# Kernel optimization log

Hardware: AMD Instinct MI355X
Metric: run time of the kernel (lower is better)

## Reference

```python
import jax, jax.numpy as jnp
import numpy as np

C = 64           # channels
CPG = 8          # channel_per_group
G = C // CPG     # offset groups = 8
K = 27           # 3x3x3 taps
N, D, H, W = 2, 8, 56, 56


def conv3d(x, w, b=None):
    y = jax.lax.conv_general_dilated(
        x, w, window_strides=(1, 1, 1), padding=[(1, 1)] * 3,
        dimension_numbers=('NCDHW', 'OIDHW', 'NCDHW'))
    if b is not None:
        y = y + b.reshape(1, -1, 1, 1, 1)
    return y


def deform_conv3d(x, off, w, groups):
    # x: [N,C,D,H,W]; off: [N, G*3*27, D,H,W]; w: [O,C,3,3,3]
    n, cin, d, h, wd = x.shape
    cpg = cin // groups
    p = d * h * wd
    off = off.reshape(n, groups, K, 3, d, h, wd)
    # kernel tap displacements in (kd,kh,kw) order, each in {-1,0,1}
    r = jnp.arange(3, dtype=x.dtype) - 1.0
    taps = jnp.stack(jnp.meshgrid(r, r, r, indexing='ij'), axis=-1).reshape(K, 3)
    gd = jnp.arange(d, dtype=x.dtype)[:, None, None]
    gh = jnp.arange(h, dtype=x.dtype)[None, :, None]
    gw = jnp.arange(wd, dtype=x.dtype)[None, None, :]
    # sampling positions [N,G,K,D,H,W]
    pd = gd + taps[:, 0][:, None, None, None] + off[:, :, :, 0]
    ph = gh + taps[:, 1][:, None, None, None] + off[:, :, :, 1]
    pw = gw + taps[:, 2][:, None, None, None] + off[:, :, :, 2]
    d0 = jnp.floor(pd); h0 = jnp.floor(ph); w0 = jnp.floor(pw)
    fd, fh, fw = pd - d0, ph - h0, pw - w0
    d0 = d0.astype(jnp.int32); h0 = h0.astype(jnp.int32); w0 = w0.astype(jnp.int32)
    xflat = x.reshape(n, groups, cpg, p)[:, :, None]  # [N,G,1,Cpg,P]
    acc = jnp.zeros((n, groups, K, cpg, p), x.dtype)
    for cd in (0, 1):
        for ch in (0, 1):
            for cw in (0, 1):
                idd, idh, idw = d0 + cd, h0 + ch, w0 + cw
                wgt = ((fd if cd else 1.0 - fd)
                       * (fh if ch else 1.0 - fh)
                       * (fw if cw else 1.0 - fw))
                valid = ((idd >= 0) & (idd < d) & (idh >= 0) & (idh < h)
                         & (idw >= 0) & (idw < wd)).astype(x.dtype)
                lin = ((jnp.clip(idd, 0, d - 1) * h + jnp.clip(idh, 0, h - 1)) * wd
                       + jnp.clip(idw, 0, wd - 1))
                g = jnp.take_along_axis(xflat, lin.reshape(n, groups, K, 1, p), axis=-1)
                acc = acc + g * (wgt * valid).reshape(n, groups, K, 1, p)
    # [N,G,K,Cpg,P] -> [N,K,C,P]
    vals = acc.transpose(0, 2, 1, 3, 4).reshape(n, K, cin, p)
    out = jnp.einsum('oik,nkip->nop', w.reshape(w.shape[0], cin, K), vals)
    return out.reshape(n, -1, d, h, wd)


def batchnorm(x, gamma, beta, eps=1e-5):
    m = x.mean((0, 2, 3, 4), keepdims=True)
    v = x.var((0, 2, 3, 4), keepdims=True)
    return (gamma.reshape(1, -1, 1, 1, 1) * (x - m) * jax.lax.rsqrt(v + eps)
            + beta.reshape(1, -1, 1, 1, 1))


def setup_inputs() -> dict:
    key = jax.random.key(0)
    ks = jax.random.split(key, 4)
    fan = C * K
    x = jax.random.normal(ks[0], (N, C, D, H, W), jnp.float32)
    w_off = jax.random.normal(ks[1], (G * 3 * K, C, 3, 3, 3), jnp.float32) * 0.01
    b_off = jnp.zeros((G * 3 * K,), jnp.float32)
    w1 = jax.random.normal(ks[2], (C, C, 3, 3, 3), jnp.float32) / np.sqrt(fan).astype(np.float32)
    w2 = jax.random.normal(ks[3], (C, C, 3, 3, 3), jnp.float32) / np.sqrt(fan).astype(np.float32)
    return dict(x=x, w_off=w_off, b_off=b_off, w1=w1,
                gamma1=jnp.ones((C,), jnp.float32), beta1=jnp.zeros((C,), jnp.float32),
                w2=w2, b2=jnp.zeros((C,), jnp.float32),
                gamma2=jnp.ones((C,), jnp.float32), beta2=jnp.zeros((C,), jnp.float32))


def reference(x, w_off, b_off, w1, gamma1, beta1, w2, b2, gamma2, beta2):
    residual = x
    off = conv3d(x, w_off, b_off)
    out = deform_conv3d(x, off, w1, G)
    out = jax.nn.relu(batchnorm(out, gamma1, beta1))
    out = conv3d(out, w2, b2)
    out = batchnorm(out, gamma2, beta2) + residual
    return jax.nn.relu(out)
```

## Files before the change

### kernel.cpp

```cpp
#include <hip/hip_runtime.h>
#include <hip/hip_bf16.h>

#define N_ 2
#define C_ 64
#define D_ 8
#define H_ 56
#define W_ 56
#define HW_ (H_*W_)
#define P_ (D_*HW_)
#define G_ 8
#define CPG_ 8
#define K_ 27
#define CO_OFF_ 648
#define MP_ 768
#define KK_ 1728
#define KB_ (KK_*2)

typedef __attribute__((ext_vector_type(8))) short shortx8;
typedef __attribute__((ext_vector_type(4))) float floatx4;
#define AS1 __attribute__((address_space(1)))
#define AS3 __attribute__((address_space(3)))

__device__ inline float b2f(unsigned short u) {
    union { unsigned u; float f; } x; x.u = ((unsigned)u) << 16; return x.f;
}
__device__ inline unsigned short f2b(float f) {
    union { float f; unsigned u; } x; x.f = f;
    unsigned r = (x.u + 0x7fffu + ((x.u >> 16) & 1u)) >> 16;
    return (unsigned short)r;
}
__device__ inline float lof(unsigned u) { union { unsigned u; float f; } x; x.u = u << 16; return x.f; }
__device__ inline float hif(unsigned u) { union { unsigned u; float f; } x; x.u = u & 0xffff0000u; return x.f; }
__device__ inline unsigned cvt_pk_bf16(float a, float b) {
    unsigned r;
    asm("v_cvt_pk_bf16_f32 %0, %1, %2" : "=v"(r) : "v"(a), "v"(b));
    return r;
}


__global__ __launch_bounds__(256) void transpose_xt_kernel(
    const float* __restrict__ x, unsigned short* __restrict__ xt)
{
    __shared__ unsigned short tile[64][65];
    int b  = blockIdx.x;
    int n  = b / (P_/64);
    int p0 = (b % (P_/64))*64;
    int tid = threadIdx.x;
    int j  = tid & 63;
    int c0 = (tid >> 6)*16;
    for (int r = 0; r < 16; ++r)
        tile[c0 + r][j] = f2b(x[((size_t)n*C_ + c0 + r)*P_ + p0 + j]);
    __syncthreads();
    unsigned* dst = (unsigned*)(xt + ((size_t)n*P_ + p0)*C_);
    #pragma unroll
    for (int it = 0; it < 8; ++it) {
        int wi  = it*256 + tid;
        int row = wi >> 5;
        int c   = (wi & 31)*2;
        unsigned lo = tile[c][row], hi = tile[c+1][row];
        dst[(size_t)row*32 + (wi & 31)] = lo | (hi << 16);
    }
}

__global__ __launch_bounds__(256) void permA1k_kernel(
    const float* __restrict__ w, unsigned short* __restrict__ A)
{
    int i = blockIdx.x*256 + threadIdx.x;
    if (i >= MP_*KK_) return;
    int m = i / KK_, r = i % KK_;
    int kk = r / 64, ci = r % 64;
    A[i] = (m < CO_OFF_) ? f2b(w[((size_t)m*C_ + ci)*K_ + kk]) : (unsigned short)0;
}

__global__ __launch_bounds__(256) void perm_w_kernel(
    const float* __restrict__ w, unsigned short* __restrict__ At)
{
    int tid = blockIdx.x*256 + threadIdx.x;
    if (tid >= C_*KK_) return;
    int o  = tid / KK_;
    int r  = tid % KK_;
    int k  = r / 64, i = r % 64;
    At[tid] = f2b(w[((size_t)o*C_ + i)*K_ + k]);
}

__global__ __launch_bounds__(256) void conv_off_fused(
    const unsigned short* __restrict__ A,
    const unsigned short* __restrict__ xt,
    const float* __restrict__ bias,
    unsigned short* __restrict__ off2)
{
    __shared__ __align__(16) short As[2][16*512];
    __shared__ __align__(16) short Bs[16*512];
    int tid = threadIdx.x;
    int w = tid >> 6, lane = tid & 63;
    int n   = blockIdx.x / 980;
    int bid = blockIdx.x % 980;
    int mt, nt;
    if (bid < 960) { int c = bid/40, r = bid%40; mt = r >> 3; nt = c*8 + (r&7); }
    else           { int r = bid - 960;          mt = r >> 2; nt = 192 + (r&3); }
    int m0 = mt*128, p0 = nt*128;
    int lm = lane & 15, lq = lane >> 4;

    const unsigned short* xtn = xt + (size_t)n*P_*C_;
    unsigned short* out2 = off2 + (size_t)n*216*P_*3;

    const char* Ab0 = (const char*)A + (size_t)(m0 + w*32 + lm)*KB_ + lq*16;
    const char* Ab1 = Ab0 + (size_t)16*KB_;

    int oct = lane & 7;
    int prj[4], dj[4], hj[4], wj[4];
    #pragma unroll
    for (int j = 0; j < 4; ++j) {
        int prow = j*32 + w*8 + (lane >> 3);
        prj[j] = prow;
        int p = p0 + prow;
        dj[j] = p / HW_;
        int hw2 = p % HW_;
        hj[j] = hw2 / W_;
        wj[j] = hw2 % W_;
    }

    auto stageA = [&](int kt, int buf) {
        __builtin_amdgcn_global_load_lds((const AS1 unsigned*)(Ab0 + kt*128),      (AS3 unsigned*)(&As[buf][(w*2)*512]),     16, 0, 0);
        __builtin_amdgcn_global_load_lds((const AS1 unsigned*)(Ab1 + kt*128),      (AS3 unsigned*)(&As[buf][(w*2+1)*512]),   16, 0, 0);
        __builtin_amdgcn_global_load_lds((const AS1 unsigned*)(Ab0 + kt*128 + 64), (AS3 unsigned*)(&As[buf][(8+w*2)*512]),   16, 0, 0);
        __builtin_amdgcn_global_load_lds((const AS1 unsigned*)(Ab1 + kt*128 + 64), (AS3 unsigned*)(&As[buf][(8+w*2+1)*512]), 16, 0, 0);
    };
    auto loadB = [&](int kt, uint4* B) {
        int kd = kt/9 - 1, kh = (kt/3)%3 - 1, kw = kt%3 - 1;
        int delta = kd*HW_ + kh*W_ + kw;
        #pragma unroll
        for (int j = 0; j < 4; ++j) {
            bool v = ((unsigned)(dj[j]+kd) < (unsigned)D_) &&
                     ((unsigned)(hj[j]+kh) < (unsigned)H_) &&
                     ((unsigned)(wj[j]+kw) < (unsigned)W_);
            uint4 val = {0u,0u,0u,0u};
            if (v) val = *(const uint4*)(xtn + (size_t)(p0 + prj[j] + delta)*C_ + oct*8);
            B[j] = val;
        }
    };

    int mh = w >> 1, nh = w & 1;
    floatx4 acc[4][4];
    #pragma unroll
    for (int i = 0; i < 4; ++i)
        #pragma unroll
        for (int j = 0; j < 4; ++j)
            acc[i][j] = (floatx4){0.f, 0.f, 0.f, 0.f};

    uint4 Bcur[4], Bnext[4];
    #pragma unroll
    for (int j = 0; j < 4; ++j) Bnext[j] = (uint4){0u,0u,0u,0u};
    stageA(0, 0);
    loadB(0, Bcur);

    for (int kt = 0; kt < 27; ++kt) {
        int buf = kt & 1;
        __syncthreads();
        #pragma unroll
        for (int j = 0; j < 4; ++j) {
            int chunk = (oct>>2)*8 + (prj[j]>>4);
            *(uint4*)&Bs[chunk*512 + ((oct&3)*16 + ((prj[j]&15) ^ oct))*8] = Bcur[j];
        }
        __syncthreads();
        if (kt < 26) { stageA(kt+1, buf^1); loadB(kt+1, Bnext); }
        #pragma unroll
        for (int ks = 0; ks < 2; ++ks) {
            int swzB = (lq*16 + (lm ^ (ks*4 + lq)))*8;
            shortx8 a[4], b[4];
            #pragma unroll
            for (int i = 0; i < 4; ++i) a[i] = *(const shortx8*)&As[buf][(ks*8 + 4*mh + i)*512 + lane*8];
            #pragma unroll
            for (int j = 0; j < 4; ++j) b[j] = *(const shortx8*)&Bs[(ks*8 + 4*nh + j)*512 + swzB];
            #pragma unroll
            for (int i = 0; i < 4; ++i)
                #pragma unroll
                for (int j = 0; j < 4; ++j)
                    acc[i][j] = __builtin_amdgcn_mfma_f32_16x16x32_bf16(a[i], b[j], acc[i][j], 0, 0, 0);
        }
        #pragma unroll
        for (int j = 0; j < 4; ++j) Bcur[j] = Bnext[j];
    }

    #pragma unroll
    for (int i = 0; i < 4; ++i) {
        int cob = m0 + (4*mh+i)*16 + lq*4;
        #pragma unroll
        for (int r = 0; r < 4; ++r) {
            int co = cob + r;
            float bv = bias[co];
            int row2 = co / 3, comp = co % 3;
            size_t base = (size_t)row2*P_*3 + comp;
            #pragma unroll
            for (int j = 0; j < 4; ++j) {
                int col = p0 + (4*nh+j)*16 + lm;
                out2[base + (size_t)col*3] = f2b(acc[i][j][r] + bv);
            }
        }
    }
}

__global__ __launch_bounds__(256) void conv_off_tail(
    const unsigned short* __restrict__ A,
    const unsigned short* __restrict__ xt,
    const float* __restrict__ bias,
    unsigned short* __restrict__ off2)
{
    __shared__ __align__(16) short As[54*512];
    __shared__ __align__(16) short Bs[16*512];
    int tid = threadIdx.x;
    int w = tid >> 6, lane = tid & 63;
    int n  = blockIdx.x / 196;
    int p0 = (blockIdx.x % 196)*128;
    int lm = lane & 15, lq = lane >> 4;

    const unsigned short* xtn = xt + (size_t)n*P_*C_;
    unsigned short* out2 = off2 + (size_t)n*216*P_*3;

    const char* Abase = (const char*)A + (size_t)(640 + lm)*KB_ + lq*16;
    for (int ch = w; ch < 54; ch += 4)
        __builtin_amdgcn_global_load_lds((const AS1 unsigned*)(Abase + ch*64),
                                         (AS3 unsigned*)(As + ch*512), 16, 0, 0);

    int oct = lane & 7;
    int prj[4], dj[4], hj[4], wj[4];
    #pragma unroll
    for (int j = 0; j < 4; ++j) {
        int prow = j*32 + w*8 + (lane >> 3);
        prj[j] = prow;
        int p = p0 + prow;
        dj[j] = p / HW_;
        int hw2 = p % HW_;
        hj[j] = hw2 / W_;
        wj[j] = hw2 % W_;
    }
    auto loadB = [&](int kt, uint4* B) {
        int kd = kt/9 - 1, kh = (kt/3)%3 - 1, kw = kt%3 - 1;
        int delta = kd*HW_ + kh*W_ + kw;
        #pragma unroll
        for (int j = 0; j < 4; ++j) {
            bool v = ((unsigned)(dj[j]+kd) < (unsigned)D_) &&
                     ((unsigned)(hj[j]+kh) < (unsigned)H_) &&
                     ((unsigned)(wj[j]+kw) < (unsigned)W_);
            uint4 val = {0u,0u,0u,0u};
            if (v) val = *(const uint4*)(xtn + (size_t)(p0 + prj[j] + delta)*C_ + oct*8);
            B[j] = val;
        }
    };

    floatx4 acc[2];
    acc[0] = (floatx4){0.f,0.f,0.f,0.f};
    acc[1] = (floatx4){0.f,0.f,0.f,0.f};

    uint4 Bcur[4], Bnext[4];
    #pragma unroll
    for (int j = 0; j < 4; ++j) Bnext[j] = (uint4){0u,0u,0u,0u};
    loadB(0, Bcur);

    for (int kt = 0; kt < 27; ++kt) {
        __syncthreads();
        #pragma unroll
        for (int j = 0; j < 4; ++j) {
            int chunk = (oct>>2)*8 + (prj[j]>>4);
            *(uint4*)&Bs[chunk*512 + ((oct&3)*16 + ((prj[j]&15) ^ oct))*8] = Bcur[j];
        }
        __syncthreads();
        if (kt < 26) loadB(kt+1, Bnext);
        #pragma unroll
        for (int ks = 0; ks < 2; ++ks) {
            int swzB = (lq*16 + (lm ^ (ks*4 + lq)))*8;
            shortx8 a = *(const shortx8*)&As[(kt*2 + ks)*512 + lane*8];
            #pragma unroll
            for (int j = 0; j < 2; ++j) {
                shortx8 b = *(const shortx8*)&Bs[(ks*8 + w*2 + j)*512 + swzB];
                acc[j] = __builtin_amdgcn_mfma_f32_16x16x32_bf16(a, b, acc[j], 0, 0, 0);
            }
        }
        #pragma unroll
        for (int j = 0; j < 4; ++j) Bcur[j] = Bnext[j];
    }

    #pragma unroll
    for (int j = 0; j < 2; ++j) {
        #pragma unroll
        for (int r = 0; r < 4; ++r) {
            int co = 640 + lq*4 + r;
            if (co < CO_OFF_) {
                int col = p0 + w*32 + j*16 + lm;
                out2[((size_t)(co/3)*P_ + col)*3 + (co%3)] = f2b(acc[j][r] + bias[co]);
            }
        }
    }
}

__global__ __launch_bounds__(256) void deform_fused(
    const unsigned short* __restrict__ xt,
    const unsigned short* __restrict__ off2,
    const unsigned short* __restrict__ A,
    unsigned short* __restrict__ y1t)
{
    __shared__ __align__(16) short SH[12288];
    int tid = threadIdx.x;
    int w = tid >> 6, lane = tid & 63;
    int n  = blockIdx.x / (P_/32);
    int p0 = (blockIdx.x % (P_/32))*32;
    int lm = lane & 15, lq = lane >> 4;

    const unsigned short* offn = off2 + (size_t)n*216*P_*3;
    const uint4* xg0 = (const uint4*)(xt + (size_t)n*P_*C_);

    const char* Ab = (const char*)A + (size_t)(w*16 + lm)*KB_ + lq*16;

    int g = lane & 7;
    int prow = tid >> 3;
    int p = p0 + prow;
    int dd = p / HW_;
    int hw2 = p % HW_;
    int hh = hw2 / W_;
    int ww = hw2 % W_;
    int bchunk = (g>>2)*2 + (prow>>4);
    int bsoff  = bchunk*512 + ((g&3)*16 + ((prow&15) ^ g))*8;

    const unsigned short* offp = offn + ((size_t)(g*K_)*P_ + p)*3;

    auto stageA = [&](int kt, int buf) {
        __builtin_amdgcn_global_load_lds((const AS1 unsigned*)(Ab + kt*128),      (AS3 unsigned*)(SH + buf*4096 + w*512),     16, 0, 0);
        __builtin_amdgcn_global_load_lds((const AS1 unsigned*)(Ab + kt*128 + 64), (AS3 unsigned*)(SH + buf*4096 + (4+w)*512), 16, 0, 0);
    };
    auto loadOff = [&](int kt, float* o) {
        const unsigned short* q = offp + (unsigned)(kt*(P_*3));
        o[0] = b2f(q[0]); o[1] = b2f(q[1]); o[2] = b2f(q[2]);
    };
    auto issueCorners = [&](int kt, const float* o, uint4* V, float* Wt) {
        int kd = kt/9 - 1, kh = (kt/3)%3 - 1, kw = kt%3 - 1;
        float pd = (float)(dd + kd) + o[0];
        float ph = (float)(hh + kh) + o[1];
        float pw = (float)(ww + kw) + o[2];
        float fd0 = floorf(pd), fh0 = floorf(ph), fw0 = floorf(pw);
        int d0 = (int)fd0, h0 = (int)fh0, w0i = (int)fw0;
        float fd = pd - fd0, fh = ph - fh0, fw = pw - fw0;
        int dc0 = min(max(d0, 0), D_-1),   dc1 = min(max(d0+1, 0), D_-1);
        int hc0 = min(max(h0, 0), H_-1),   hc1 = min(max(h0+1, 0), H_-1);
        int wc0 = min(max(w0i, 0), W_-1),  wc1 = min(max(w0i+1, 0), W_-1);
        float wd0 = ((unsigned)d0      < (unsigned)D_) ? 1.f - fd : 0.f;
        float wd1 = ((unsigned)(d0+1)  < (unsigned)D_) ? fd       : 0.f;
        float wh0 = ((unsigned)h0      < (unsigned)H_) ? 1.f - fh : 0.f;
        float wh1 = ((unsigned)(h0+1)  < (unsigned)H_) ? fh       : 0.f;
        Wt[4] = ((unsigned)w0i     < (unsigned)W_) ? 1.f - fw : 0.f;
        Wt[5] = ((unsigned)(w0i+1) < (unsigned)W_) ? fw       : 0.f;
        Wt[0] = wd0*wh0; Wt[1] = wd0*wh1; Wt[2] = wd1*wh0; Wt[3] = wd1*wh1;
        unsigned rb00 = (unsigned)((dc0*H_ + hc0)*W_)*8u + (unsigned)g;
        unsigned rb01 = (unsigned)((dc0*H_ + hc1)*W_)*8u + (unsigned)g;
        unsigned rb10 = (unsigned)((dc1*H_ + hc0)*W_)*8u + (unsigned)g;
        unsigned rb11 = (unsigned)((dc1*H_ + hc1)*W_)*8u + (unsigned)g;
        unsigned c0 = (unsigned)wc0*8u, c1 = (unsigned)wc1*8u;
        V[0] = xg0[rb00 + c0];
        V[1] = xg0[rb00 + c1];
        V[2] = xg0[rb01 + c0];
        V[3] = xg0[rb01 + c1];
        V[4] = xg0[rb10 + c0];
        V[5] = xg0[rb10 + c1];
        V[6] = xg0[rb11 + c0];
        V[7] = xg0[rb11 + c1];
    };
    auto reduceStore = [&](const uint4* V, const float* Wt, int half) {
        float res[8];
        #pragma unroll
        for (int c = 0; c < 8; ++c) res[c] = 0.f;
        #pragma unroll
        for (int c = 0; c < 8; ++c) {
            uint4 v4 = V[c];
            float wgt = Wt[c>>1] * ((c & 1) ? Wt[5] : Wt[4]);
            res[0] = fmaf(wgt, lof(v4.x), res[0]);
            res[1] = fmaf(wgt, hif(v4.x), res[1]);
            res[2] = fmaf(wgt, lof(v4.y), res[2]);
            res[3] = fmaf(wgt, hif(v4.y), res[3]);
            res[4] = fmaf(wgt, lof(v4.z), res[4]);
            res[5] = fmaf(wgt, hif(v4.z), res[5]);
            res[6] = fmaf(wgt, lof(v4.w), res[6]);
            res[7] = fmaf(wgt, hif(v4.w), res[7]);
        }
        uint4 o4;
        o4.x = cvt_pk_bf16(res[0], res[1]);
        o4.y = cvt_pk_bf16(res[2], res[3]);
        o4.z = cvt_pk_bf16(res[4], res[5]);
        o4.w = cvt_pk_bf16(res[6], res[7]);
        *(uint4*)&SH[8192 + half*2048 + bsoff] = o4;
    };

    int mh = w >> 1, nh = w & 1;
    floatx4 acc[2];
    acc[0] = (floatx4){0.f,0.f,0.f,0.f};
    acc[1] = (floatx4){0.f,0.f,0.f,0.f};

    auto doMFMA = [&](int buf) {
        #pragma unroll
        for (int ks = 0; ks < 2; ++ks) {
            int swzB = (lq*16 + (lm ^ (ks*4 + lq)))*8;
            shortx8 b = *(const shortx8*)&SH[8192 + buf*2048 + (ks*2 + nh)*512 + swzB];
            #pragma unroll
            for (int i = 0; i < 2; ++i) {
                shortx8 a = *(const shortx8*)&SH[buf*4096 + (ks*4 + 2*mh+i)*512 + lane*8];
                acc[i] = __builtin_amdgcn_mfma_f32_16x16x32_bf16(a, b, acc[i], 0, 0, 0);
            }
        }
    };

    uint4 VA[8], VB[8];
    float WA[6], WB[6];
    float oC[3], oD[3], oE[3], oF[3];

    stageA(0, 0);
    {
        float o0[3], o1[3];
        loadOff(0, o0); loadOff(1, o1); loadOff(2, oC); loadOff(3, oD);
        issueCorners(0, o0, VA, WA);
        issueCorners(1, o1, VB, WB);
        reduceStore(VA, WA, 0);
    }

    for (int kt = 0; kt < 26; kt += 2) {
        __syncthreads();
        stageA(kt+1, 1);
        issueCorners(kt+2, oC, VA, WA);
        if (kt+4 <= 26) loadOff(kt+4, oE);
        doMFMA(0);
        reduceStore(VB, WB, 1);

        __syncthreads();
        stageA(kt+2, 0);
        if (kt+3 <= 26) issueCorners(kt+3, oD, VB, WB);
        if (kt+5 <= 26) loadOff(kt+5, oF);
        doMFMA(1);
        reduceStore(VA, WA, 0);

        oC[0]=oE[0]; oC[1]=oE[1]; oC[2]=oE[2];
        oD[0]=oF[0]; oD[1]=oF[1]; oD[2]=oF[2];
    }
    __syncthreads();
    doMFMA(0);

    __syncthreads();
    #pragma unroll
    for (int i = 0; i < 2; ++i) {
        int ob = mh*32 + i*16 + lq*4;
        int pc = nh*16 + lm;
        #pragma unroll
        for (int rr = 0; rr < 4; ++rr)
            SH[pc*72 + ob + rr] = (short)f2b(acc[i][rr]);
    }
    __syncthreads();
    {
        int row = tid >> 3, seg = tid & 7;
        uint4 v = *(const uint4*)&SH[row*72 + seg*8];
        *(uint4*)(y1t + ((size_t)n*P_ + p0 + row)*C_ + seg*8) = v;
    }
}

__global__ __launch_bounds__(256) void conv2_fused(
    const unsigned short* __restrict__ y1t,
    const float* __restrict__ st1,
    const unsigned short* __restrict__ A,
    const float* __restrict__ bias,
    unsigned short* __restrict__ y2)
{
    __shared__ __align__(16) short As[2][4096];
    __shared__ float sc[64], sf[64];
    int tid = threadIdx.x;
    if (tid < 64) sc[tid] = st1[tid];
    else if (tid < 128) sf[tid-64] = st1[tid];
    int w = tid >> 6, lane = tid & 63;
    int n  = blockIdx.x / (P_/64);
    int p0 = (blockIdx.x % (P_/64))*64;
    int lm = lane & 15, lq = lane >> 4;

    const unsigned short* y1n = y1t + (size_t)n*P_*C_;
    unsigned short* y2n = y2 + (size_t)n*C_*P_;
    const char* Ab = (const char*)A + (size_t)(w*16 + lm)*KB_ + lq*16;

    int p = p0 + w*16 + lm;
    int dd = p / HW_, hw2 = p % HW_;
    int hh = hw2 / W_, ww = hw2 % W_;

    auto stageA = [&](int kt, int buf) {
        __builtin_amdgcn_global_load_lds((const AS1 unsigned*)(Ab + kt*128),      (AS3 unsigned*)(&As[buf][w*512]),     16, 0, 0);
        __builtin_amdgcn_global_load_lds((const AS1 unsigned*)(Ab + kt*128 + 64), (AS3 unsigned*)(&As[buf][(4+w)*512]), 16, 0, 0);
    };
    auto issueV = [&](int kt, uint4* V, int& M) {
        int kd = kt/9 - 1, kh = (kt/3)%3 - 1, kw = kt%3 - 1;
        int delta = kd*HW_ + kh*W_ + kw;
        bool v = ((unsigned)(dd+kd) < (unsigned)D_) &&
                 ((unsigned)(hh+kh) < (unsigned)H_) &&
                 ((unsigned)(ww+kw) < (unsigned)W_);
        M = v ? 1 : 0;
        #pragma unroll
        for (int ks = 0; ks < 2; ++ks) {
            uint4 val = {0u,0u,0u,0u};
            if (v) val = *(const uint4*)(y1n + (size_t)(p + delta)*C_ + (ks*4 + lq)*8);
            V[ks] = val;
        }
    };
    auto reduceT = [&](uint4 V, int ks, int M) -> shortx8 {
        uint4 o4 = {0u,0u,0u,0u};
        if (M) {
            int cb = (ks*4 + lq)*8;
            float r0 = fmaxf(lof(V.x)*sc[cb+0] + sf[cb+0], 0.f);
            float r1 = fmaxf(hif(V.x)*sc[cb+1] + sf[cb+1], 0.f);
            float r2 = fmaxf(lof(V.y)*sc[cb+2] + sf[cb+2], 0.f);
            float r3 = fmaxf(hif(V.y)*sc[cb+3] + sf[cb+3], 0.f);
            float r4 = fmaxf(lof(V.z)*sc[cb+4] + sf[cb+4], 0.f);
            float r5 = fmaxf(hif(V.z)*sc[cb+5] + sf[cb+5], 0.f);
            float r6 = fmaxf(lof(V.w)*sc[cb+6] + sf[cb+6], 0.f);
            float r7 = fmaxf(hif(V.w)*sc[cb+7] + sf[cb+7], 0.f);
            o4.x = cvt_pk_bf16(r0, r1);
            o4.y = cvt_pk_bf16(r2, r3);
            o4.z = cvt_pk_bf16(r4, r5);
            o4.w = cvt_pk_bf16(r6, r7);
        }
        return *(shortx8*)&o4;
    };

    floatx4 acc[4];
    #pragma unroll
    for (int i = 0; i < 4; ++i) acc[i] = (floatx4){0.f,0.f,0.f,0.f};

    uint4 V[2];
    int M;
    stageA(0, 0);
    issueV(0, V, M);

    for (int kt = 0; kt < 27; ++kt) {
        int buf = kt & 1;
        __syncthreads();
        if (kt < 26) stageA(kt+1, buf^1);
        shortx8 b0 = reduceT(V[0], 0, M);
        shortx8 b1 = reduceT(V[1], 1, M);
        if (kt < 26) issueV(kt+1, V, M);
        #pragma unroll
        for (int i = 0; i < 4; ++i) {
            shortx8 a = *(const shortx8*)&As[buf][(0*4 + i)*512 + lane*8];
            acc[i] = __builtin_amdgcn_mfma_f32_16x16x32_bf16(a, b0, acc[i], 0, 0, 0);
        }
        #pragma unroll
        for (int i = 0; i < 4; ++i) {
            shortx8 a = *(const shortx8*)&As[buf][(1*4 + i)*512 + lane*8];
            acc[i] = __builtin_amdgcn_mfma_f32_16x16x32_bf16(a, b1, acc[i], 0, 0, 0);
        }
    }

    #pragma unroll
    for (int i = 0; i < 4; ++i) {
        #pragma unroll
        for (int r = 0; r < 4; ++r) {
            int co = i*16 + lq*4 + r;
            y2n[(size_t)co*P_ + p] = f2b(acc[i][r] + bias[co]);
        }
    }
}

__global__ __launch_bounds__(256) void stats_partial_kernel(
    const unsigned short* __restrict__ y1t, float* __restrict__ part)
{
    int b = blockIdx.x, tid = threadIdx.x;
    int c = tid & 63, sub = tid >> 6;
    float s = 0.f, q = 0.f;
    for (int rr = 0; rr < 128; ++rr) {
        int row = b*512 + sub*128 + rr;
        float v = b2f(y1t[(size_t)row*C_ + c]);
        s += v;
        q = fmaf(v, v, q);
    }
    __shared__ float ss[256], qq[256];
    ss[tid] = s; qq[tid] = q;
    __syncthreads();
    if (tid < 64) {
        float S = ss[tid] + ss[64+tid] + ss[128+tid] + ss[192+tid];
        float Q = qq[tid] + qq[64+tid] + qq[128+tid] + qq[192+tid];
        part[b*128 + tid]      = S;
        part[b*128 + 64 + tid] = Q;
    }
}

__global__ void stats_final_kernel(
    const float* __restrict__ part,
    const float* __restrict__ gamma, const float* __restrict__ beta,
    float* __restrict__ st1)
{
    int c = threadIdx.x;
    float S = 0.f, Q = 0.f;
    for (int b = 0; b < 98; ++b) {
        S += part[b*128 + c];
        Q += part[b*128 + 64 + c];
    }
    const float inv = 1.f / (float)(N_*P_);
    float m = S * inv;
    float var = Q * inv - m*m;
    float scale = rsqrtf(var + 1e-5f) * gamma[c];
    st1[c]      = scale;
    st1[64 + c] = beta[c] - m*scale;
}

__global__ __launch_bounds__(256) void bn_stats_kernel(
    const unsigned short* __restrict__ src, float* __restrict__ stats)
{
    int c   = blockIdx.x;
    int tid = threadIdx.x;
    float s = 0.f, q = 0.f;
    for (int n = 0; n < N_; ++n) {
        const unsigned short* p = src + ((size_t)n*C_ + c)*P_;
        for (int i = tid; i < P_; i += 256) {
            float v = b2f(p[i]);
            s += v;
            q = fmaf(v, v, q);
        }
    }
    #pragma unroll
    for (int o = 32; o; o >>= 1) {
        s += __shfl_down(s, o);
        q += __shfl_down(q, o);
    }
    __shared__ float sh[2][4];
    int wave = tid >> 6;
    if ((tid & 63) == 0) { sh[0][wave] = s; sh[1][wave] = q; }
    __syncthreads();
    if (tid == 0) {
        float S = sh[0][0] + sh[0][1] + sh[0][2] + sh[0][3];
        float Q = sh[1][0] + sh[1][1] + sh[1][2] + sh[1][3];
        const float inv = 1.f / (float)(N_*P_);
        float m  = S * inv;
        float var = Q * inv - m*m;
        stats[c]      = m;
        stats[C_ + c] = rsqrtf(var + 1e-5f);
    }
}

__global__ __launch_bounds__(256) void bn_add_relu_kernel(
    const unsigned short* __restrict__ y2, const float* __restrict__ x,
    const float* __restrict__ stats,
    const float* __restrict__ gamma, const float* __restrict__ beta,
    float* __restrict__ out)
{
    size_t idx = (size_t)blockIdx.x*256 + threadIdx.x;
    int c = (int)((idx / P_) % C_);
    float v = (b2f(y2[idx]) - stats[c]) * stats[C_ + c] * gamma[c] + beta[c] + x[idx];
    out[idx] = fmaxf(v, 0.f);
}

extern "C" void kernel_launch(void* const* d_in, const int* in_sizes, int n_in,
                              void* d_out, int out_size, void* d_ws, size_t ws_size,
                              hipStream_t stream) {
    const float* x     = (const float*)d_in[0];
    const float* w_off = (const float*)d_in[1];
    const float* b_off = (const float*)d_in[2];
    const float* w1    = (const float*)d_in[3];
    const float* g1    = (const float*)d_in[4];
    const float* be1   = (const float*)d_in[5];
    const float* w2    = (const float*)d_in[6];
    const float* b2    = (const float*)d_in[7];
    const float* g2    = (const float*)d_in[8];
    const float* be2   = (const float*)d_in[9];
    float* out = (float*)d_out;

    float* st1  = (float*)d_ws;
    float* st2  = st1 + 128;
    float* part = st2 + 128;
    unsigned short* off2 = (unsigned short*)(part + 98*128);
    unsigned short* xt  = off2 + (size_t)N_*216*P_*3;
    unsigned short* y1t = xt  + (size_t)N_*P_*C_;
    unsigned short* y2  = y1t + (size_t)N_*P_*C_;
    unsigned short* A1k = y2  + (size_t)N_*C_*P_;
    unsigned short* A1t = A1k + (size_t)MP_*KK_;
    unsigned short* A2t = A1t + (size_t)C_*KK_;

    transpose_xt_kernel<<<N_*(P_/64), 256, 0, stream>>>(x, xt);
    permA1k_kernel<<<(MP_*KK_+255)/256, 256, 0, stream>>>(w_off, A1k);
    perm_w_kernel<<<(C_*KK_+255)/256, 256, 0, stream>>>(w1, A1t);
    perm_w_kernel<<<(C_*KK_+255)/256, 256, 0, stream>>>(w2, A2t);

    conv_off_fused<<<2*980, 256, 0, stream>>>(A1k, xt, b_off, off2);
    conv_off_tail<<<2*196, 256, 0, stream>>>(A1k, xt, b_off, off2);

    deform_fused<<<N_*(P_/32), 256, 0, stream>>>(xt, off2, A1t, y1t);

    stats_partial_kernel<<<98, 256, 0, stream>>>(y1t, part);
    stats_final_kernel<<<1, 64, 0, stream>>>(part, g1, be1, st1);

    conv2_fused<<<N_*(P_/64), 256, 0, stream>>>(y1t, st1, A2t, b2, y2);

    bn_stats_kernel<<<C_, 256, 0, stream>>>(y2, st2);
    bn_add_relu_kernel<<<(N_*C_*P_)/256, 256, 0, stream>>>(y2, x, st2, g2, be2, out);
}
```

Before: 538.1 us.

## Remove LDS staging and per-tap barriers; split K across waves in deform conv

In deform_fused, the sampled B fragment now stays in registers and feeds MFMA directly, and the weight A fragments are read straight from global memory instead of being staged through LDS. The waves split the channel-group (K) dimension and the two halves are summed through shared memory at the end. conv2_fused likewise drops LDS staging of weights and its per-tap __syncthreads, and double-buffers its input loads. This removes the barriers and LDS traffic inside the tap loop, at the cost of repeated global/L2 reads of weights per wave and a final cross-wave reduction.

```diff
diff --git a/kernel.cpp b/kernel.cpp
--- a/kernel.cpp
+++ b/kernel.cpp
@@ -299,34 +299,28 @@
     const unsigned short* __restrict__ A,
     unsigned short* __restrict__ y1t)
 {
-    __shared__ __align__(16) short SH[12288];
+    __shared__ __align__(16) float SXF[2][64][17];
+    __shared__ __align__(16) short SHT[32*72];
     int tid = threadIdx.x;
     int w = tid >> 6, lane = tid & 63;
+    int ksh = w >> 1, nh = w & 1;
+    int lm = lane & 15, lq = lane >> 4;
     int n  = blockIdx.x / (P_/32);
     int p0 = (blockIdx.x % (P_/32))*32;
-    int lm = lane & 15, lq = lane >> 4;
-
-    const unsigned short* offn = off2 + (size_t)n*216*P_*3;
-    const uint4* xg0 = (const uint4*)(xt + (size_t)n*P_*C_);
-
-    const char* Ab = (const char*)A + (size_t)(w*16 + lm)*KB_ + lq*16;
-
-    int g = lane & 7;
-    int prow = tid >> 3;
-    int p = p0 + prow;
+
+    int g  = ksh*4 + lq;
+    int pl = nh*16 + lm;
+    int p  = p0 + pl;
     int dd = p / HW_;
     int hw2 = p % HW_;
     int hh = hw2 / W_;
     int ww = hw2 % W_;
-    int bchunk = (g>>2)*2 + (prow>>4);
-    int bsoff  = bchunk*512 + ((g&3)*16 + ((prow&15) ^ g))*8;
-
+
+    const unsigned short* offn = off2 + (size_t)n*216*P_*3;
+    const uint4* xg0 = (const uint4*)(xt + (size_t)n*P_*C_);
     const unsigned short* offp = offn + ((size_t)(g*K_)*P_ + p)*3;
-
-    auto stageA = [&](int kt, int buf) {
-        __builtin_amdgcn_global_load_lds((const AS1 unsigned*)(Ab + kt*128),      (AS3 unsigned*)(SH + buf*4096 + w*512),     16, 0, 0);
-        __builtin_amdgcn_global_load_lds((const AS1 unsigned*)(Ab + kt*128 + 64), (AS3 unsigned*)(SH + buf*4096 + (4+w)*512), 16, 0, 0);
-    };
+    const unsigned short* Arow = A + (size_t)lm*KK_ + ksh*32 + lq*8;
+
     auto loadOff = [&](int kt, float* o) {
         const unsigned short* q = offp + (unsigned)(kt*(P_*3));
         o[0] = b2f(q[0]); o[1] = b2f(q[1]); o[2] = b2f(q[2]);
@@ -363,7 +357,12 @@
         V[6] = xg0[rb11 + c0];
         V[7] = xg0[rb11 + c1];
     };
-    auto reduceStore = [&](const uint4* V, const float* Wt, int half) {
+
+    floatx4 acc[4];
+    #pragma unroll
+    for (int i = 0; i < 4; ++i) acc[i] = (floatx4){0.f,0.f,0.f,0.f};
+
+    auto computeTap = [&](int kt, const uint4* V, const float* Wt) {
         float res[8];
         #pragma unroll
         for (int c = 0; c < 8; ++c) res[c] = 0.f;
@@ -385,74 +384,55 @@
         o4.y = cvt_pk_bf16(res[2], res[3]);
         o4.z = cvt_pk_bf16(res[4], res[5]);
         o4.w = cvt_pk_bf16(res[6], res[7]);
-        *(uint4*)&SH[8192 + half*2048 + bsoff] = o4;
-    };
-
-    int mh = w >> 1, nh = w & 1;
-    floatx4 acc[2];
-    acc[0] = (floatx4){0.f,0.f,0.f,0.f};
-    acc[1] = (floatx4){0.f,0.f,0.f,0.f};
-
-    auto doMFMA = [&](int buf) {
-        #pragma unroll
-        for (int ks = 0; ks < 2; ++ks) {
-            int swzB = (lq*16 + (lm ^ (ks*4 + lq)))*8;
-            shortx8 b = *(const shortx8*)&SH[8192 + buf*2048 + (ks*2 + nh)*512 + swzB];
-            #pragma unroll
-            for (int i = 0; i < 2; ++i) {
-                shortx8 a = *(const shortx8*)&SH[buf*4096 + (ks*4 + 2*mh+i)*512 + lane*8];
-                acc[i] = __builtin_amdgcn_mfma_f32_16x16x32_bf16(a, b, acc[i], 0, 0, 0);
-            }
+        shortx8 b = *(shortx8*)&o4;
+        #pragma unroll
+        for (int i = 0; i < 4; ++i) {
+            shortx8 a = *(const shortx8*)(Arow + (size_t)i*16*KK_ + kt*64);
+            acc[i] = __builtin_amdgcn_mfma_f32_16x16x32_bf16(a, b, acc[i], 0, 0, 0);
         }
     };
 
     uint4 VA[8], VB[8];
     float WA[6], WB[6];
-    float oC[3], oD[3], oE[3], oF[3];
-
-    stageA(0, 0);
-    {
-        float o0[3], o1[3];
-        loadOff(0, o0); loadOff(1, o1); loadOff(2, oC); loadOff(3, oD);
-        issueCorners(0, o0, VA, WA);
-        issueCorners(1, o1, VB, WB);
-        reduceStore(VA, WA, 0);
-    }
+    float oA[3], oB[3];
+
+    loadOff(0, oA);
+    loadOff(1, oB);
+    issueCorners(0, oA, VA, WA);
 
     for (int kt = 0; kt < 26; kt += 2) {
-        __syncthreads();
-        stageA(kt+1, 1);
-        issueCorners(kt+2, oC, VA, WA);
-        if (kt+4 <= 26) loadOff(kt+4, oE);
-        doMFMA(0);
-        reduceStore(VB, WB, 1);
-
-        __syncthreads();
-        stageA(kt+2, 0);
-        if (kt+3 <= 26) issueCorners(kt+3, oD, VB, WB);
-        if (kt+5 <= 26) loadOff(kt+5, oF);
-        doMFMA(1);
-        reduceStore(VA, WA, 0);
-
-        oC[0]=oE[0]; oC[1]=oE[1]; oC[2]=oE[2];
-        oD[0]=oF[0]; oD[1]=oF[1]; oD[2]=oF[2];
-    }
+        issueCorners(kt+1, oB, VB, WB);
+        loadOff(kt+2, oA);
+        computeTap(kt, VA, WA);
+        issueCorners(kt+2, oA, VA, WA);
+        if (kt+3 <= 26) loadOff(kt+3, oB);
+        computeTap(kt+1, VB, WB);
+    }
+    computeTap(26, VA, WA);
+
     __syncthreads();
-    doMFMA(0);
-
+    if (ksh == 1) {
+        #pragma unroll
+        for (int i = 0; i < 4; ++i)
+            #pragma unroll
+            for (int r = 0; r < 4; ++r)
+                SXF[nh][i*16 + lq*4 + r][lm] = acc[i][r];
+    }
     __syncthreads();
-    #pragma unroll
-    for (int i = 0; i < 2; ++i) {
-        int ob = mh*32 + i*16 + lq*4;
-        int pc = nh*16 + lm;
-        #pragma unroll
-        for (int rr = 0; rr < 4; ++rr)
-            SH[pc*72 + ob + rr] = (short)f2b(acc[i][rr]);
+    if (ksh == 0) {
+        #pragma unroll
+        for (int i = 0; i < 4; ++i) {
+            #pragma unroll
+            for (int r = 0; r < 4; ++r) {
+                float v = acc[i][r] + SXF[nh][i*16 + lq*4 + r][lm];
+                SHT[pl*72 + i*16 + lq*4 + r] = (short)f2b(v);
+            }
+        }
     }
     __syncthreads();
     {
         int row = tid >> 3, seg = tid & 7;
-        uint4 v = *(const uint4*)&SH[row*72 + seg*8];
+        uint4 v = *(const uint4*)&SHT[row*72 + seg*8];
         *(uint4*)(y1t + ((size_t)n*P_ + p0 + row)*C_ + seg*8) = v;
     }
 }
@@ -464,11 +444,11 @@
     const float* __restrict__ bias,
     unsigned short* __restrict__ y2)
 {
-    __shared__ __align__(16) short As[2][4096];
     __shared__ float sc[64], sf[64];
     int tid = threadIdx.x;
     if (tid < 64) sc[tid] = st1[tid];
     else if (tid < 128) sf[tid-64] = st1[tid];
+    __syncthreads();
     int w = tid >> 6, lane = tid & 63;
     int n  = blockIdx.x / (P_/64);
     int p0 = (blockIdx.x % (P_/64))*64;
@@ -476,16 +456,12 @@
 
     const unsigned short* y1n = y1t + (size_t)n*P_*C_;
     unsigned short* y2n = y2 + (size_t)n*C_*P_;
-    const char* Ab = (const char*)A + (size_t)(w*16 + lm)*KB_ + lq*16;
+    const unsigned short* Arow = A + (size_t)lm*KK_ + lq*8;
 
     int p = p0 + w*16 + lm;
     int dd = p / HW_, hw2 = p % HW_;
     int hh = hw2 / W_, ww = hw2 % W_;
 
-    auto stageA = [&](int kt, int buf) {
-        __builtin_amdgcn_global_load_lds((const AS1 unsigned*)(Ab + kt*128),      (AS3 unsigned*)(&As[buf][w*512]),     16, 0, 0);
-        __builtin_amdgcn_global_load_lds((const AS1 unsigned*)(Ab + kt*128 + 64), (AS3 unsigned*)(&As[buf][(4+w)*512]), 16, 0, 0);
-    };
     auto issueV = [&](int kt, uint4* V, int& M) {
         int kd = kt/9 - 1, kh = (kt/3)%3 - 1, kw = kt%3 - 1;
         int delta = kd*HW_ + kh*W_ + kw;
@@ -524,29 +500,33 @@
     #pragma unroll
     for (int i = 0; i < 4; ++i) acc[i] = (floatx4){0.f,0.f,0.f,0.f};
 
-    uint4 V[2];
-    int M;
-    stageA(0, 0);
-    issueV(0, V, M);
-
-    for (int kt = 0; kt < 27; ++kt) {
-        int buf = kt & 1;
-        __syncthreads();
-        if (kt < 26) stageA(kt+1, buf^1);
+    auto computeTap = [&](int kt, const uint4* V, int M) {
         shortx8 b0 = reduceT(V[0], 0, M);
         shortx8 b1 = reduceT(V[1], 1, M);
-        if (kt < 26) issueV(kt+1, V, M);
         #pragma unroll
         for (int i = 0; i < 4; ++i) {
-            shortx8 a = *(const shortx8*)&As[buf][(0*4 + i)*512 + lane*8];
+            shortx8 a = *(const shortx8*)(Arow + (size_t)i*16*KK_ + kt*64);
             acc[i] = __builtin_amdgcn_mfma_f32_16x16x32_bf16(a, b0, acc[i], 0, 0, 0);
         }
         #pragma unroll
         for (int i = 0; i < 4; ++i) {
-            shortx8 a = *(const shortx8*)&As[buf][(1*4 + i)*512 + lane*8];
+            shortx8 a = *(const shortx8*)(Arow + (size_t)i*16*KK_ + kt*64 + 32);
             acc[i] = __builtin_amdgcn_mfma_f32_16x16x32_bf16(a, b1, acc[i], 0, 0, 0);
         }
-    }
+    };
+
+    uint4 VA[2], VB[2];
+    int MA, MB;
+    issueV(0, VA, MA);
+    issueV(1, VB, MB);
+
+    for (int kt = 0; kt < 26; kt += 2) {
+        computeTap(kt, VA, MA);
+        issueV(kt+2, VA, MA);
+        computeTap(kt+1, VB, MB);
+        if (kt+3 <= 26) issueV(kt+3, VB, MB);
+    }
+    computeTap(26, VA, MA);
 
     #pragma unroll
     for (int i = 0; i < 4; ++i) {
```

Result: slower. 699.5 us (+30.0%).
